# Kernel optimization log

Hardware: AMD Instinct MI355X
Metric: run time of the kernel (lower is better)

The kernel has to match this reference:

```python
import jax, jax.numpy as jnp
import numpy as np

NEG_SLOPE = 0.2


def setup_inputs() -> dict:
    key = jax.random.key(0)
    ks = jax.random.split(key, 12)
    Nm, Na, E, Din, H, D = 50000, 50000, 400000, 128, 8, 32
    return {
        "master_feats": jax.random.normal(ks[0], (Nm, Din), jnp.float32),
        "attn_feats0": jax.random.normal(ks[1], (Na, Din), jnp.float32),
        "attn_feats1": jax.random.normal(ks[2], (Na, Din), jnp.float32),
        "src0": jax.random.randint(ks[3], (E,), 0, Na, jnp.int32),
        "dst0": jax.random.randint(ks[4], (E,), 0, Nm, jnp.int32),
        "src1": jax.random.randint(ks[5], (E,), 0, Na, jnp.int32),
        "dst1": jax.random.randint(ks[6], (E,), 0, Nm, jnp.int32),
        "W_master": jax.random.normal(ks[7], (Din, H * D), jnp.float32) * 0.08,
        "W0": jax.random.normal(ks[8], (Din, H * D), jnp.float32) * 0.08,
        "W1": jax.random.normal(ks[9], (Din, H * D), jnp.float32) * 0.08,
        "attn_l": jax.random.normal(ks[10], (H, D), jnp.float32) * 0.1,
        "attn_r": jax.random.normal(ks[11], (H, D), jnp.float32) * 0.1,
    }


def reference(master_feats, attn_feats0, attn_feats1, src0, dst0, src1, dst1,
              W_master, W0, W1, attn_l, attn_r):
    Nm = master_feats.shape[0]
    H, D = attn_l.shape

    # Per-node-type linear projections (no bias) + attention logits.
    ft_m = (master_feats @ W_master).reshape(Nm, H, D)        # [Nm,H,D]
    er = jnp.einsum("nhd,hd->nh", ft_m, attn_r)               # [Nm,H]

    def proj(feats, W):
        ft = (feats @ W).reshape(feats.shape[0], H, D)
        el = jnp.einsum("nhd,hd->nh", ft, attn_l)
        return ft, el

    ft0, el0 = proj(attn_feats0, W0)
    ft1, el1 = proj(attn_feats1, W1)

    lrelu = lambda x: jnp.where(x >= 0, x, NEG_SLOPE * x)
    e0 = lrelu(el0[src0] + er[dst0])                          # [E0,H]
    e1 = lrelu(el1[src1] + er[dst1])                          # [E1,H]

    # Heterograph edge softmax: normalize over ALL incoming edges of each
    # master node, regardless of source node type (subtract dst-max for
    # stability; mathematically identical to the conditional path in source).
    dst = jnp.concatenate([dst0, dst1])
    e = jnp.concatenate([e0, e1], axis=0)                     # [E0+E1,H]
    emax = jax.ops.segment_max(e, dst, num_segments=Nm)
    emax = jnp.where(jnp.isfinite(emax), emax, 0.0)           # nodes w/o edges
    ee = jnp.exp(e - emax[dst])
    esum = jax.ops.segment_sum(ee, dst, num_segments=Nm)
    a = ee / esum[dst]                                        # [E0+E1,H]

    # u_mul_e + sum aggregation onto master nodes.
    E0 = src0.shape[0]
    msg = jnp.concatenate(
        [ft0[src0] * a[:E0, :, None], ft1[src1] * a[E0:, :, None]], axis=0
    )                                                         # [E,H,D]
    rst = jax.ops.segment_sum(msg, dst, num_segments=Nm)      # [Nm,H,D]
    return rst
```

## Files before the change

### kernel.cpp

```cpp
#include <hip/hip_runtime.h>
#include <cstdint>
#include <cstddef>

#define NEG_SLOPE 0.2f

typedef __attribute__((ext_vector_type(8))) short short8;
typedef __attribute__((ext_vector_type(4))) float f32x4;

static __device__ __forceinline__ unsigned short f2bf(float x) {
  uint32_t u = __float_as_uint(x);
  uint32_t r = (u + 0x7FFFu + ((u >> 16) & 1u)) >> 16;
  return (unsigned short)r;
}
static __device__ __forceinline__ float bf2f(unsigned short b) {
  return __uint_as_float(((uint32_t)b) << 16);
}

__global__ void wt_kernel(const float* __restrict__ W0, const float* __restrict__ W1,
                          const float* __restrict__ W2,
                          unsigned short* __restrict__ T0, unsigned short* __restrict__ T1,
                          unsigned short* __restrict__ T2) {
  const float* W = (blockIdx.y == 0) ? W0 : (blockIdx.y == 1) ? W1 : W2;
  unsigned short* T = (blockIdx.y == 0) ? T0 : (blockIdx.y == 1) ? T1 : T2;
  int c = blockIdx.x * 2 + (threadIdx.x >> 7);
  int k = threadIdx.x & 127;
  T[c * 128 + k] = f2bf(W[k * 256 + c]);
}

__global__ __launch_bounds__(256)
void proj_mfma_kernel(const float* __restrict__ fm, const float* __restrict__ fa0,
                      const float* __restrict__ fa1,
                      const unsigned short* __restrict__ Wtm,
                      const unsigned short* __restrict__ Wt0,
                      const unsigned short* __restrict__ Wt1,
                      const float* __restrict__ attn_l, const float* __restrict__ attn_r,
                      int Nm, int Na0, int Na1,
                      unsigned short* __restrict__ ft_all, float* __restrict__ el_all,
                      float* __restrict__ er) {
  const int z = blockIdx.z;
  const float* feats = (z == 0) ? fm : (z == 1) ? fa0 : fa1;
  const unsigned short* Wt = (z == 0) ? Wtm : (z == 1) ? Wt0 : Wt1;
  const float* av = (z == 0) ? attn_r : attn_l;
  const int N = (z == 0) ? Nm : (z == 1) ? Na0 : Na1;
  unsigned short* ft_out = (z == 0) ? nullptr
                         : (z == 1) ? ft_all : ft_all + (size_t)Na0 * 256;
  float* el_out = (z == 0) ? er : (z == 1) ? el_all : el_all + (size_t)Na0 * 8;

  const int rb = blockIdx.x * 128;
  if (rb >= N) return;

  __shared__ unsigned short As[128 * 128];
  __shared__ unsigned short Bs[128 * 128];
  const int t = threadIdx.x;

  #pragma unroll
  for (int it = 0; it < 16; ++it) {
    int i = it * 256 + t;
    int r = i >> 5, kc = (i & 31) << 2;
    float4 f = make_float4(0.f, 0.f, 0.f, 0.f);
    if (rb + r < N) f = *(const float4*)(&feats[(size_t)(rb + r) * 128 + kc]);
    ushort4 u;
    u.x = f2bf(f.x); u.y = f2bf(f.y); u.z = f2bf(f.z); u.w = f2bf(f.w);
    uint32_t byte = ((uint32_t)(r * 256 + kc * 2)) ^ ((uint32_t)((r & 7) << 4));
    *(ushort4*)((char*)As + byte) = u;
  }
  __syncthreads();

  const int wid = t >> 6, lane = t & 63;
  const int wm = wid >> 1, wn = wid & 1;
  const int l15 = lane & 15, l4 = lane >> 4;

  short8 af[4][4];
  #pragma unroll
  for (int kb = 0; kb < 4; ++kb)
    #pragma unroll
    for (int mf = 0; mf < 4; ++mf) {
      int row = wm * 64 + mf * 16 + l15;
      uint32_t byte = ((uint32_t)(row * 256 + kb * 64 + l4 * 16)) ^ ((uint32_t)((row & 7) << 4));
      af[kb][mf] = *(const short8*)((const char*)As + byte);
    }

  #pragma unroll
  for (int cbi = 0; cbi < 2; ++cbi) {
    const int cb = cbi * 128;
    __syncthreads();
    #pragma unroll
    for (int it = 0; it < 8; ++it) {
      int i = it * 256 + t;
      int c = i >> 4, k8 = (i & 15) << 3;
      short8 w = *(const short8*)(&Wt[(size_t)(cb + c) * 128 + k8]);
      uint32_t byte = ((uint32_t)(c * 256 + k8 * 2)) ^ ((uint32_t)((c & 7) << 4));
      *(short8*)((char*)Bs + byte) = w;
    }
    __syncthreads();

    f32x4 acc[4][4];
    #pragma unroll
    for (int a = 0; a < 4; ++a)
      #pragma unroll
      for (int b = 0; b < 4; ++b)
        acc[a][b] = (f32x4){0.f, 0.f, 0.f, 0.f};

    #pragma unroll
    for (int kb = 0; kb < 4; ++kb) {
      short8 bf[4];
      #pragma unroll
      for (int nf = 0; nf < 4; ++nf) {
        int col = wn * 64 + nf * 16 + l15;
        uint32_t byte = ((uint32_t)(col * 256 + kb * 64 + l4 * 16)) ^ ((uint32_t)((col & 7) << 4));
        bf[nf] = *(const short8*)((const char*)Bs + byte);
      }
      #pragma unroll
      for (int mf = 0; mf < 4; ++mf)
        #pragma unroll
        for (int nf = 0; nf < 4; ++nf)
          acc[mf][nf] = __builtin_amdgcn_mfma_f32_16x16x32_bf16(af[kb][mf], bf[nf], acc[mf][nf], 0, 0, 0);
    }

    const int head0 = cbi * 4 + wn * 2;
    float avv[4];
    #pragma unroll
    for (int nf = 0; nf < 4; ++nf)
      avv[nf] = av[(head0 + (nf >> 1)) * 32 + (nf & 1) * 16 + l15];

    #pragma unroll
    for (int mf = 0; mf < 4; ++mf) {
      const int rowb = rb + wm * 64 + mf * 16;
      #pragma unroll
      for (int hh = 0; hh < 2; ++hh) {
        float v[4];
        #pragma unroll
        for (int reg = 0; reg < 4; ++reg) {
          float p = fmaf(acc[mf][2 * hh][reg], avv[2 * hh],
                         acc[mf][2 * hh + 1][reg] * avv[2 * hh + 1]);
          p += __shfl_xor(p, 1);
          p += __shfl_xor(p, 2);
          p += __shfl_xor(p, 4);
          p += __shfl_xor(p, 8);
          v[reg] = p;
        }
        if (l15 < 4) {
          int row = rowb + l4 * 4 + l15;
          if (row < N) {
            float val = (l15 == 0) ? v[0] : (l15 == 1) ? v[1] : (l15 == 2) ? v[2] : v[3];
            el_out[(size_t)row * 8 + head0 + hh] = val;
          }
        }
      }
    }

    if (ft_out != nullptr) {
      __syncthreads();
      #pragma unroll
      for (int mf = 0; mf < 4; ++mf)
        #pragma unroll
        for (int nf = 0; nf < 4; ++nf)
          #pragma unroll
          for (int reg = 0; reg < 4; ++reg) {
            int row = wm * 64 + mf * 16 + l4 * 4 + reg;
            int colb = (wn * 64 + nf * 16 + l15) * 2;
            uint32_t byte = ((uint32_t)(row * 256 + colb)) ^ ((uint32_t)((row & 7) << 4));
            *(unsigned short*)((char*)As + byte) = f2bf(acc[mf][nf][reg]);
          }
      __syncthreads();
      #pragma unroll
      for (int it = 0; it < 8; ++it) {
        int i = it * 256 + t;
        int r = i >> 4, j = i & 15;
        int pj = j ^ (r & 7);
        short8 vv = *(const short8*)((const char*)As + r * 256 + pj * 16);
        if (rb + r < N)
          *(short8*)(&ft_out[(size_t)(rb + r) * 256 + cb + j * 8]) = vv;
      }
    }
  }
}

__global__ void count_deg_kernel(const int* __restrict__ dst0, int E0,
                                 const int* __restrict__ dst1, int E1,
                                 int* __restrict__ deg) {
  int E = E0 + E1;
  for (int i = blockIdx.x * blockDim.x + threadIdx.x; i < E;
       i += gridDim.x * blockDim.x) {
    int d = (i < E0) ? dst0[i] : dst1[i - E0];
    atomicAdd(&deg[d], 1);
  }
}

__global__ __launch_bounds__(1024)
void block_reduce_kernel(const int* __restrict__ deg, int* __restrict__ partial, int n) {
  __shared__ int wsum[16];
  const int t = threadIdx.x;
  int idx = blockIdx.x * 1024 + t;
  int v = (idx < n) ? deg[idx] : 0;
  #pragma unroll
  for (int off = 1; off < 64; off <<= 1) v += __shfl_xor(v, off);
  if ((t & 63) == 0) wsum[t >> 6] = v;
  __syncthreads();
  if (t < 16) {
    int x = wsum[t];
    #pragma unroll
    for (int off = 1; off < 16; off <<= 1) x += __shfl_xor(x, off);
    if (t == 0) partial[blockIdx.x] = x;
  }
}

__global__ __launch_bounds__(64)
void partial_scan_kernel(const int* __restrict__ partial, int* __restrict__ base,
                         int nb, int* __restrict__ offs, int n) {
  const int t = threadIdx.x;
  int v = (t < nb) ? partial[t] : 0;
  int incl = v;
  #pragma unroll
  for (int off = 1; off < 64; off <<= 1) {
    int x = __shfl_up(incl, off);
    if (t >= off) incl += x;
  }
  if (t < nb) base[t] = incl - v;
  if (t == nb - 1) offs[n] = incl;
}

__global__ __launch_bounds__(1024)
void apply_scan_kernel(const int* __restrict__ deg, const int* __restrict__ base,
                       int* __restrict__ offs, int* __restrict__ cursor, int n) {
  __shared__ int wsum[16];
  const int t = threadIdx.x;
  const int idx = blockIdx.x * 1024 + t;
  int v = (idx < n) ? deg[idx] : 0;
  const int lane = t & 63, w = t >> 6;
  int incl = v;
  #pragma unroll
  for (int off = 1; off < 64; off <<= 1) {
    int x = __shfl_up(incl, off);
    if (lane >= off) incl += x;
  }
  if (lane == 63) wsum[w] = incl;
  __syncthreads();
  if (t < 16) {
    int x = wsum[t];
    #pragma unroll
    for (int off = 1; off < 16; off <<= 1) {
      int y = __shfl_up(x, off);
      if (t >= off) x += y;
    }
    wsum[t] = x;
  }
  __syncthreads();
  int excl = base[blockIdx.x] + ((w > 0) ? wsum[w - 1] : 0) + incl - v;
  if (idx < n) {
    offs[idx] = excl;
    cursor[idx] = excl;
  }
}

__global__ void scatter_kernel(const int* __restrict__ src0, const int* __restrict__ dst0, int E0,
                               const int* __restrict__ src1, const int* __restrict__ dst1, int E1,
                               int* __restrict__ cursor, int* __restrict__ slots,
                               uint4* __restrict__ wslots,
                               const float* __restrict__ el, const float* __restrict__ er,
                               int Na0) {
  int E = E0 + E1;
  for (int i = blockIdx.x * blockDim.x + threadIdx.x; i < E;
       i += gridDim.x * blockDim.x) {
    int s, d;
    if (i < E0) { s = src0[i]; d = dst0[i]; }
    else        { s = src1[i - E0] + Na0; d = dst1[i - E0]; }
    int pos = atomicAdd(&cursor[d], 1);
    slots[pos] = s;

    const float* elp = &el[(size_t)s * 8];
    const float* erp = &er[(size_t)d * 8];
    float4 ea = *(const float4*)elp, eb = *(const float4*)(elp + 4);
    float4 ra = *(const float4*)erp, rb = *(const float4*)(erp + 4);
    float w[8];
    w[0] = ea.x + ra.x; w[1] = ea.y + ra.y; w[2] = ea.z + ra.z; w[3] = ea.w + ra.w;
    w[4] = eb.x + rb.x; w[5] = eb.y + rb.y; w[6] = eb.z + rb.z; w[7] = eb.w + rb.w;
    uint4 pk;
    uint32_t* pku = (uint32_t*)&pk;
    #pragma unroll
    for (int q = 0; q < 4; ++q) {
      float v0 = w[2 * q], v1 = w[2 * q + 1];
      v0 = fmaxf(v0, NEG_SLOPE * v0);
      v1 = fmaxf(v1, NEG_SLOPE * v1);
      uint32_t b0 = f2bf(__expf(v0)), b1 = f2bf(__expf(v1));
      pku[q] = b0 | (b1 << 16);
    }
    wslots[pos] = pk;
  }
}

__global__ __launch_bounds__(256)
void aggregate_kernel(const int* __restrict__ offs, const int* __restrict__ slots,
                      const unsigned short* __restrict__ wsl,
                      const unsigned short* __restrict__ ft,
                      float* __restrict__ rst, int Nm) {
  int gid = blockIdx.x * blockDim.x + threadIdx.x;
  int n = gid >> 6;
  int lane = threadIdx.x & 63;
  if (n >= Nm) return;
  int beg = offs[n], end = offs[n + 1];
  int h = lane >> 3;
  float o0 = 0.f, o1 = 0.f, o2 = 0.f, o3 = 0.f;
  if (beg < end) {
    float sw = 0.f;
    float w0 = 0.f, w1 = 0.f, w2 = 0.f, w3 = 0.f, w4 = 0.f, w5 = 0.f, w6 = 0.f, w7 = 0.f;
    ushort4 f0 = {0,0,0,0}, f1 = f0, f2 = f0, f3 = f0, f4 = f0, f5 = f0, f6 = f0, f7 = f0;

#define LD(idx, ww, ff)                                                          \
    do {                                                                         \
      if ((idx) < end) {                                                         \
        ww = bf2f(wsl[(size_t)(uint32_t)(idx) * 8 + h]);                         \
        int s_ = slots[(idx)];                                                   \
        ff = *(const ushort4*)((const char*)ft +                                 \
                               (((size_t)(uint32_t)s_) << 9) + lane * 8);        \
      }                                                                          \
    } while (0)

#define PR(ww, ff)                                                               \
    do {                                                                         \
      sw += ww;                                                                  \
      o0 = fmaf(ww, bf2f(ff.x), o0);                                             \
      o1 = fmaf(ww, bf2f(ff.y), o1);                                             \
      o2 = fmaf(ww, bf2f(ff.z), o2);                                             \
      o3 = fmaf(ww, bf2f(ff.w), o3);                                             \
    } while (0)

    LD(beg + 0, w0, f0); LD(beg + 1, w1, f1); LD(beg + 2, w2, f2); LD(beg + 3, w3, f3);
    LD(beg + 4, w4, f4); LD(beg + 5, w5, f5); LD(beg + 6, w6, f6); LD(beg + 7, w7, f7);

    for (int i = beg; i < end; i += 8) {
      PR(w0, f0); LD(i + 8, w0, f0);
      if (i + 1 < end) { PR(w1, f1); LD(i + 9,  w1, f1); }
      if (i + 2 < end) { PR(w2, f2); LD(i + 10, w2, f2); }
      if (i + 3 < end) { PR(w3, f3); LD(i + 11, w3, f3); }
      if (i + 4 < end) { PR(w4, f4); LD(i + 12, w4, f4); }
      if (i + 5 < end) { PR(w5, f5); LD(i + 13, w5, f5); }
      if (i + 6 < end) { PR(w6, f6); LD(i + 14, w6, f6); }
      if (i + 7 < end) { PR(w7, f7); LD(i + 15, w7, f7); }
    }
#undef LD
#undef PR
    float inv = 1.0f / sw;
    o0 *= inv; o1 *= inv; o2 *= inv; o3 *= inv;
  }
  *(float4*)(&rst[(size_t)n * 256 + lane * 4]) = make_float4(o0, o1, o2, o3);
}

extern "C" void kernel_launch(void* const* d_in, const int* in_sizes, int n_in,
                              void* d_out, int out_size, void* d_ws, size_t ws_size,
                              hipStream_t stream) {
  const float* master = (const float*)d_in[0];
  const float* af0    = (const float*)d_in[1];
  const float* af1    = (const float*)d_in[2];
  const int*   src0   = (const int*)d_in[3];
  const int*   dst0   = (const int*)d_in[4];
  const int*   src1   = (const int*)d_in[5];
  const int*   dst1   = (const int*)d_in[6];
  const float* Wm     = (const float*)d_in[7];
  const float* W0     = (const float*)d_in[8];
  const float* W1     = (const float*)d_in[9];
  const float* attn_l = (const float*)d_in[10];
  const float* attn_r = (const float*)d_in[11];

  const int Nm  = in_sizes[0] / 128;
  const int Na0 = in_sizes[1] / 128;
  const int Na1 = in_sizes[2] / 128;
  const int E0  = in_sizes[3];
  const int E1  = in_sizes[5];
  float* rst = (float*)d_out;

  char* ws = (char*)d_ws;
  size_t off = 0;
  auto alloc = [&](size_t b) -> char* {
    char* p = ws + off;
    off += (b + 511) & ~(size_t)511;
    return p;
  };
  unsigned short* ft = (unsigned short*)alloc((size_t)(Na0 + Na1) * 256 * sizeof(unsigned short));
  float* el = (float*)alloc((size_t)(Na0 + Na1) * 8 * sizeof(float));
  float* er = (float*)alloc((size_t)Nm * 8 * sizeof(float));
  unsigned short* Wtm = (unsigned short*)alloc(256 * 128 * sizeof(unsigned short));
  unsigned short* Wt0 = (unsigned short*)alloc(256 * 128 * sizeof(unsigned short));
  unsigned short* Wt1 = (unsigned short*)alloc(256 * 128 * sizeof(unsigned short));
  int* deg     = (int*)alloc((size_t)Nm * sizeof(int));
  int* offs    = (int*)alloc((size_t)(Nm + 1) * sizeof(int));
  int* cursor  = (int*)alloc((size_t)Nm * sizeof(int));
  int* partial = (int*)alloc(64 * sizeof(int));
  int* pbase   = (int*)alloc(64 * sizeof(int));
  int* slots   = (int*)alloc((size_t)(E0 + E1) * sizeof(int));
  uint4* wslots = (uint4*)alloc((size_t)(E0 + E1) * sizeof(uint4));

  wt_kernel<<<dim3(128, 3), 256, 0, stream>>>(Wm, W0, W1, Wtm, Wt0, Wt1);

  int Nmax = Nm > Na0 ? Nm : Na0; if (Na1 > Nmax) Nmax = Na1;
  const int mb = (Nmax + 127) / 128;
  proj_mfma_kernel<<<dim3(mb, 1, 3), 256, 0, stream>>>(
      master, af0, af1, Wtm, Wt0, Wt1, attn_l, attn_r,
      Nm, Na0, Na1, ft, el, er);

  hipMemsetAsync(deg, 0, (size_t)Nm * sizeof(int), stream);
  count_deg_kernel<<<1024, 256, 0, stream>>>(dst0, E0, dst1, E1, deg);
  const int nb = (Nm + 1023) / 1024;
  block_reduce_kernel<<<nb, 1024, 0, stream>>>(deg, partial, Nm);
  partial_scan_kernel<<<1, 64, 0, stream>>>(partial, pbase, nb, offs, Nm);
  apply_scan_kernel<<<nb, 1024, 0, stream>>>(deg, pbase, offs, cursor, Nm);
  scatter_kernel<<<1024, 256, 0, stream>>>(src0, dst0, E0, src1, dst1, E1,
                                           cursor, slots, wslots, el, er, Na0);

  aggregate_kernel<<<(Nm + 3) / 4, 256, 0, stream>>>(offs, slots,
                                                     (const unsigned short*)wslots,
                                                     ft, rst, Nm);
}
```

Baseline: 256.8 us.

## Load GEMM operands directly to registers and compute transposed MFMA, dropping LDS staging

The projection GEMM no longer stages the feature tile and weight tile through shared memory. Each lane loads its fp32 A fragments and bf16 B fragments straight from global memory into registers. The MFMA operands are swapped so each lane's accumulator holds contiguous output columns of one node row. That layout lets the ft output be written directly as ushort4 without an LDS transpose, and shortens the attention-logit reduction to two shuffles. The intent is to remove the LDS round trips and block barriers, at the cost of less coalesced global loads and redundant weight fetches across waves.

```diff
diff --git a/kernel.cpp b/kernel.cpp
--- a/kernel.cpp
+++ b/kernel.cpp
@@ -49,50 +49,45 @@
   const int rb = blockIdx.x * 128;
   if (rb >= N) return;
 
-  __shared__ unsigned short As[128 * 128];
-  __shared__ unsigned short Bs[128 * 128];
   const int t = threadIdx.x;
-
-  #pragma unroll
-  for (int it = 0; it < 16; ++it) {
-    int i = it * 256 + t;
-    int r = i >> 5, kc = (i & 31) << 2;
-    float4 f = make_float4(0.f, 0.f, 0.f, 0.f);
-    if (rb + r < N) f = *(const float4*)(&feats[(size_t)(rb + r) * 128 + kc]);
-    ushort4 u;
-    u.x = f2bf(f.x); u.y = f2bf(f.y); u.z = f2bf(f.z); u.w = f2bf(f.w);
-    uint32_t byte = ((uint32_t)(r * 256 + kc * 2)) ^ ((uint32_t)((r & 7) << 4));
-    *(ushort4*)((char*)As + byte) = u;
-  }
-  __syncthreads();
-
   const int wid = t >> 6, lane = t & 63;
   const int wm = wid >> 1, wn = wid & 1;
   const int l15 = lane & 15, l4 = lane >> 4;
 
+  const int arow = rb + wm * 64 + l15;
   short8 af[4][4];
   #pragma unroll
-  for (int kb = 0; kb < 4; ++kb)
-    #pragma unroll
-    for (int mf = 0; mf < 4; ++mf) {
-      int row = wm * 64 + mf * 16 + l15;
-      uint32_t byte = ((uint32_t)(row * 256 + kb * 64 + l4 * 16)) ^ ((uint32_t)((row & 7) << 4));
-      af[kb][mf] = *(const short8*)((const char*)As + byte);
-    }
+  for (int mf = 0; mf < 4; ++mf) {
+    int row = arow + mf * 16;
+    const float* rp = &feats[(size_t)row * 128];
+    bool ok = row < N;
+    #pragma unroll
+    for (int kb = 0; kb < 4; ++kb) {
+      float4 lo = make_float4(0.f, 0.f, 0.f, 0.f), hi = lo;
+      if (ok) {
+        lo = *(const float4*)(rp + kb * 32 + l4 * 8);
+        hi = *(const float4*)(rp + kb * 32 + l4 * 8 + 4);
+      }
+      short8 v;
+      v[0] = f2bf(lo.x); v[1] = f2bf(lo.y); v[2] = f2bf(lo.z); v[3] = f2bf(lo.w);
+      v[4] = f2bf(hi.x); v[5] = f2bf(hi.y); v[6] = f2bf(hi.z); v[7] = f2bf(hi.w);
+      af[kb][mf] = v;
+    }
+  }
 
   #pragma unroll
   for (int cbi = 0; cbi < 2; ++cbi) {
-    const int cb = cbi * 128;
-    __syncthreads();
-    #pragma unroll
-    for (int it = 0; it < 8; ++it) {
-      int i = it * 256 + t;
-      int c = i >> 4, k8 = (i & 15) << 3;
-      short8 w = *(const short8*)(&Wt[(size_t)(cb + c) * 128 + k8]);
-      uint32_t byte = ((uint32_t)(c * 256 + k8 * 2)) ^ ((uint32_t)((c & 7) << 4));
-      *(short8*)((char*)Bs + byte) = w;
-    }
-    __syncthreads();
+    const int cbw = cbi * 128 + wn * 64;
+    const int head0 = cbw >> 5;
+
+    short8 bf[4][4];
+    #pragma unroll
+    for (int nf = 0; nf < 4; ++nf) {
+      const unsigned short* wp = &Wt[(size_t)(cbw + nf * 16 + l15) * 128];
+      #pragma unroll
+      for (int kb = 0; kb < 4; ++kb)
+        bf[kb][nf] = *(const short8*)(wp + kb * 32 + l4 * 8);
+    }
 
     f32x4 acc[4][4];
     #pragma unroll
@@ -102,75 +97,47 @@
         acc[a][b] = (f32x4){0.f, 0.f, 0.f, 0.f};
 
     #pragma unroll
-    for (int kb = 0; kb < 4; ++kb) {
-      short8 bf[4];
-      #pragma unroll
-      for (int nf = 0; nf < 4; ++nf) {
-        int col = wn * 64 + nf * 16 + l15;
-        uint32_t byte = ((uint32_t)(col * 256 + kb * 64 + l4 * 16)) ^ ((uint32_t)((col & 7) << 4));
-        bf[nf] = *(const short8*)((const char*)Bs + byte);
-      }
+    for (int kb = 0; kb < 4; ++kb)
       #pragma unroll
       for (int mf = 0; mf < 4; ++mf)
         #pragma unroll
         for (int nf = 0; nf < 4; ++nf)
-          acc[mf][nf] = __builtin_amdgcn_mfma_f32_16x16x32_bf16(af[kb][mf], bf[nf], acc[mf][nf], 0, 0, 0);
-    }
-
-    const int head0 = cbi * 4 + wn * 2;
-    float avv[4];
+          acc[mf][nf] = __builtin_amdgcn_mfma_f32_16x16x32_bf16(
+              bf[kb][nf], af[kb][mf], acc[mf][nf], 0, 0, 0);
+
+    float avf[4][4];
     #pragma unroll
     for (int nf = 0; nf < 4; ++nf)
-      avv[nf] = av[(head0 + (nf >> 1)) * 32 + (nf & 1) * 16 + l15];
+      #pragma unroll
+      for (int reg = 0; reg < 4; ++reg)
+        avf[nf][reg] = av[(head0 + (nf >> 1)) * 32 + (nf & 1) * 16 + l4 * 4 + reg];
 
     #pragma unroll
     for (int mf = 0; mf < 4; ++mf) {
-      const int rowb = rb + wm * 64 + mf * 16;
+      int node = arow + mf * 16;
+      bool ok = node < N;
+      if (ft_out != nullptr && ok) {
+        size_t base = (size_t)node * 256 + cbw + l4 * 4;
+        #pragma unroll
+        for (int nf = 0; nf < 4; ++nf) {
+          ushort4 u;
+          u.x = f2bf(acc[mf][nf][0]); u.y = f2bf(acc[mf][nf][1]);
+          u.z = f2bf(acc[mf][nf][2]); u.w = f2bf(acc[mf][nf][3]);
+          *(ushort4*)(&ft_out[base + nf * 16]) = u;
+        }
+      }
       #pragma unroll
       for (int hh = 0; hh < 2; ++hh) {
-        float v[4];
+        float p = 0.f;
         #pragma unroll
         for (int reg = 0; reg < 4; ++reg) {
-          float p = fmaf(acc[mf][2 * hh][reg], avv[2 * hh],
-                         acc[mf][2 * hh + 1][reg] * avv[2 * hh + 1]);
-          p += __shfl_xor(p, 1);
-          p += __shfl_xor(p, 2);
-          p += __shfl_xor(p, 4);
-          p += __shfl_xor(p, 8);
-          v[reg] = p;
+          p = fmaf(acc[mf][2 * hh][reg], avf[2 * hh][reg], p);
+          p = fmaf(acc[mf][2 * hh + 1][reg], avf[2 * hh + 1][reg], p);
         }
-        if (l15 < 4) {
-          int row = rowb + l4 * 4 + l15;
-          if (row < N) {
-            float val = (l15 == 0) ? v[0] : (l15 == 1) ? v[1] : (l15 == 2) ? v[2] : v[3];
-            el_out[(size_t)row * 8 + head0 + hh] = val;
-          }
-        }
-      }
-    }
-
-    if (ft_out != nullptr) {
-      __syncthreads();
-      #pragma unroll
-      for (int mf = 0; mf < 4; ++mf)
-        #pragma unroll
-        for (int nf = 0; nf < 4; ++nf)
-          #pragma unroll
-          for (int reg = 0; reg < 4; ++reg) {
-            int row = wm * 64 + mf * 16 + l4 * 4 + reg;
-            int colb = (wn * 64 + nf * 16 + l15) * 2;
-            uint32_t byte = ((uint32_t)(row * 256 + colb)) ^ ((uint32_t)((row & 7) << 4));
-            *(unsigned short*)((char*)As + byte) = f2bf(acc[mf][nf][reg]);
-          }
-      __syncthreads();
-      #pragma unroll
-      for (int it = 0; it < 8; ++it) {
-        int i = it * 256 + t;
-        int r = i >> 4, j = i & 15;
-        int pj = j ^ (r & 7);
-        short8 vv = *(const short8*)((const char*)As + r * 256 + pj * 16);
-        if (rb + r < N)
-          *(short8*)(&ft_out[(size_t)(rb + r) * 256 + cb + j * 8]) = vv;
+        p += __shfl_xor(p, 16);
+        p += __shfl_xor(p, 32);
+        if (ok && l4 == 0)
+          el_out[(size_t)node * 8 + head0 + hh] = p;
       }
     }
   }
```

After: 241.8 us. 5.8% less time.
